# Performance work log

Hardware: AMD Instinct MI355X
Metric: run time of the kernel (lower is better)

Reference implementation:

```python
import jax, jax.numpy as jnp
import numpy as np

B, C, H, W, K = 8, 768, 64, 64, 256
EPS = 1e-12  # torch F.normalize eps


def setup_inputs() -> dict:
    key = jax.random.key(0)
    k1, k2 = jax.random.split(key)
    return {
        "x": jax.random.normal(k1, (B, C, H, W), dtype=jnp.float32),
        "centroids": jax.random.normal(k2, (B, C, K), dtype=jnp.float32),
        "sim_alpha": jnp.ones((1,), dtype=jnp.float32),
        "sim_beta": jnp.zeros((1,), dtype=jnp.float32),
    }


def reference(x, centroids, sim_alpha, sim_beta):
    b, c, h, w = x.shape
    n = h * w
    x_r = x.reshape(b, c, n)               # (B,C,N)
    xt = jnp.swapaxes(x_r, 1, 2)           # (B,N,C) tokens
    ct = jnp.swapaxes(centroids, 1, 2)     # (B,K,C) centroids
    # cosine similarity (F.normalize uses max(norm, eps))
    xn = xt / jnp.maximum(jnp.linalg.norm(xt, axis=-1, keepdims=True), EPS)
    cn = ct / jnp.maximum(jnp.linalg.norm(ct, axis=-1, keepdims=True), EPS)
    cos = jnp.einsum('bkc,bnc->bkn', cn, xn)                  # (B,K,N)
    sim = jax.nn.sigmoid(sim_beta + sim_alpha * cos)          # (B,K,N)
    # hard assignment mask: each token kept only for its argmax centroid
    max_idx = jnp.argmax(sim, axis=1)                         # (B,N)
    mask = jnp.swapaxes(jax.nn.one_hot(max_idx, sim.shape[1], dtype=sim.dtype), 1, 2)  # (B,K,N)
    sim_masked = sim * mask                                   # (B,K,N)
    # aggregation: sum over tokens weighted by masked similarity
    agg = jnp.einsum('bkn,bnc->bkc', sim_masked, xt)          # (B,K,C)
    counts = jnp.sum(mask, axis=-1, keepdims=True)            # (B,K,1)
    hyperedges = (agg + ct) / (counts + 1.0)                  # (B,K,C)
    return hyperedges, sim_masked
```

## Files before the change

### kernel.cpp

```cpp
#include <hip/hip_runtime.h>
#include <cmath>

#define Bdim 8
#define Cdim 768
#define Kdim 256
#define Ndim 4096
#define NT 64
#define KC2 32
#define NCH (Cdim / KC2)
#define CB2 4
#define NCOPY 4

typedef __bf16 bf16x8 __attribute__((ext_vector_type(8)));
typedef short  s16x8  __attribute__((ext_vector_type(8)));
typedef float  f32x4  __attribute__((ext_vector_type(4)));
union U8 { s16x8 s; bf16x8 b; };

typedef __attribute__((address_space(1))) const unsigned int g_u32;
typedef __attribute__((address_space(3))) unsigned int l_u32;
__device__ __forceinline__ void gload16(const void* g, void* l) {
    __builtin_amdgcn_global_load_lds((g_u32*)g, (l_u32*)l, 16, 0, 0);
}

__device__ __forceinline__ unsigned short bf16_rne(float f) {
    unsigned u = __float_as_uint(f);
    unsigned r = u + 0x7FFFu + ((u >> 16) & 1u);
    return (unsigned short)(r >> 16);
}
__device__ __forceinline__ float bf2f(unsigned short h) {
    return __uint_as_float((unsigned)h << 16);
}

__device__ __forceinline__ void lds_fadd_nc(float* p, float v) {
    auto lp = (__attribute__((address_space(3))) float*)p;
    asm volatile("ds_add_f32 %0, %1"
                 :: "v"((unsigned)(unsigned long long)lp), "v"(v));
}

__device__ __forceinline__ void split3(float v, short& h, short& m, short& l) {
    unsigned u = __float_as_uint(v);
    unsigned th = u + 0x7FFFu + ((u >> 16) & 1u);
    h = (short)(th >> 16);
    float r1 = v - __uint_as_float(th & 0xFFFF0000u);
    unsigned u1 = __float_as_uint(r1);
    unsigned tm = u1 + 0x7FFFu + ((u1 >> 16) & 1u);
    m = (short)(tm >> 16);
    float r2 = r1 - __uint_as_float(tm & 0xFFFF0000u);
    unsigned u2 = __float_as_uint(r2);
    unsigned tl = u2 + 0x7FFFu + ((u2 >> 16) & 1u);
    l = (short)(tl >> 16);
}

__global__ __launch_bounds__(256) void prep_kernel(
    const float* __restrict__ cents, float* __restrict__ invc, int* __restrict__ cnt)
{
    __shared__ float red[4][Kdim];
    const int tid = threadIdx.x;
    const int b = blockIdx.x;
    const float* cb = cents + (size_t)b * Cdim * Kdim;
    const int q = tid & 63, g = tid >> 6;
    float4 ss = make_float4(0.f, 0.f, 0.f, 0.f);
    for (int r = g; r < Cdim; r += 4) {
        float4 v = *(const float4*)(cb + (size_t)r * Kdim + q * 4);
        ss.x = fmaf(v.x, v.x, ss.x); ss.y = fmaf(v.y, v.y, ss.y);
        ss.z = fmaf(v.z, v.z, ss.z); ss.w = fmaf(v.w, v.w, ss.w);
    }
    *(float4*)&red[g][q * 4] = ss;
    __syncthreads();
    float s = red[0][tid] + red[1][tid] + red[2][tid] + red[3][tid];
    invc[b * Kdim + tid] = 1.f / fmaxf(sqrtf(s), 1e-12f);
    cnt[b * Kdim + tid] = 0;
}

__global__ __launch_bounds__(256) void cvt_kernel(
    const float* __restrict__ cents, short* __restrict__ centH,
    short* __restrict__ centM, short* __restrict__ centL)
{
    const int k = threadIdx.x;
    const int bc = blockIdx.x;
    const float* src = cents + ((size_t)(bc / 96) * Cdim + (size_t)(bc % 96) * 8) * Kdim + k;
    s16x8 H, M, L;
    #pragma unroll
    for (int e = 0; e < 8; ++e) {
        short h, m, l;
        split3(src[(size_t)e * Kdim], h, m, l);
        H[e] = h; M[e] = m; L[e] = l;
    }
    ((s16x8*)centH)[(size_t)bc * 256 + k] = H;
    ((s16x8*)centM)[(size_t)bc * 256 + k] = M;
    ((s16x8*)centL)[(size_t)bc * 256 + k] = L;
}

__global__ __launch_bounds__(256) void xpose_kernel(
    const float* __restrict__ x, unsigned short* __restrict__ xTh)
{
    __shared__ float tile[64][68];
    const int tid = threadIdx.x;
    const int bid = blockIdx.x;
    const int b  = bid / (12 * 64);
    const int r  = bid % (12 * 64);
    const int ct = r / 64, nt = r % 64;
    const float* src = x + ((size_t)b * Cdim + ct * 64) * Ndim + nt * 64;
    #pragma unroll
    for (int it = 0; it < 4; ++it) {
        int idx = tid + it * 256;
        int c = idx >> 4, n4 = idx & 15;
        float4 v = *(const float4*)&src[(size_t)c * Ndim + n4 * 4];
        *(float4*)&tile[c][n4 * 4] = v;
    }
    __syncthreads();
    #pragma unroll
    for (int it = 0; it < 8; ++it) {
        int idx = tid + it * 256;
        int n = idx >> 5, cp = idx & 31;
        unsigned pk = (unsigned)bf16_rne(tile[cp * 2][n])
                    | ((unsigned)bf16_rne(tile[cp * 2 + 1][n]) << 16);
        *(unsigned*)&xTh[((size_t)(b * Ndim + nt * 64 + n)) * Cdim + ct * 64 + cp * 2] = pk;
    }
}

__global__ __launch_bounds__(256) void scan_kernel(
    const int* __restrict__ cnt, const int* __restrict__ kArr,
    int* __restrict__ bucketOff, int* __restrict__ toks)
{
    __shared__ int cS[256];
    __shared__ int offS[256];
    __shared__ int cur[256];
    const int tid = threadIdx.x;
    const int b = blockIdx.x;
    cS[tid] = cnt[b * 256 + tid];
    __syncthreads();
    if (tid == 0) {
        int a = 0;
        for (int k = 0; k < 256; ++k) { offS[k] = a; a += cS[k]; }
    }
    __syncthreads();
    bucketOff[b * 256 + tid] = offS[tid];
    cur[tid] = offS[tid];
    __syncthreads();
    for (int i = tid; i < Ndim; i += 256) {
        int k = kArr[b * Ndim + i];
        int pos = atomicAdd(&cur[k], 1);
        toks[b * Ndim + pos] = i;
    }
}

__global__ __launch_bounds__(192) void aggB_kernel(
    const unsigned short* __restrict__ xTh,
    const float* __restrict__ cents,
    const float* __restrict__ wArr,
    const int* __restrict__ toks,
    const int* __restrict__ bucketOff,
    const int* __restrict__ cnt,
    float* __restrict__ hyp)
{
    const int tid = threadIdx.x;
    const int b  = blockIdx.x >> 7;
    const int kg = blockIdx.x & 127;
    const int t4 = tid * 4;
    #pragma unroll
    for (int j = 0; j < 2; ++j) {
        const int k = kg * 2 + j;
        const int off = bucketOff[b * 256 + k];
        const int num = cnt[b * 256 + k];
        const int base = b * Ndim + off;
        float a0 = 0.f, a1 = 0.f, a2 = 0.f, a3 = 0.f;
        int i = 0;
        for (; i + 4 <= num; i += 4) {
            int na = toks[base + i],     nb = toks[base + i + 1];
            int nc = toks[base + i + 2], nd = toks[base + i + 3];
            float wa = wArr[b * Ndim + na], wb = wArr[b * Ndim + nb];
            float wc = wArr[b * Ndim + nc], wd = wArr[b * Ndim + nd];
            ushort4 ha = *(const ushort4*)&xTh[((size_t)(b * Ndim + na)) * Cdim + t4];
            ushort4 hb = *(const ushort4*)&xTh[((size_t)(b * Ndim + nb)) * Cdim + t4];
            ushort4 hc = *(const ushort4*)&xTh[((size_t)(b * Ndim + nc)) * Cdim + t4];
            ushort4 hd = *(const ushort4*)&xTh[((size_t)(b * Ndim + nd)) * Cdim + t4];
            a0 += wa * bf2f(ha.x) + wb * bf2f(hb.x) + wc * bf2f(hc.x) + wd * bf2f(hd.x);
            a1 += wa * bf2f(ha.y) + wb * bf2f(hb.y) + wc * bf2f(hc.y) + wd * bf2f(hd.y);
            a2 += wa * bf2f(ha.z) + wb * bf2f(hb.z) + wc * bf2f(hc.z) + wd * bf2f(hd.z);
            a3 += wa * bf2f(ha.w) + wb * bf2f(hb.w) + wc * bf2f(hc.w) + wd * bf2f(hd.w);
        }
        for (; i < num; ++i) {
            int n = toks[base + i];
            float w = wArr[b * Ndim + n];
            ushort4 h = *(const ushort4*)&xTh[((size_t)(b * Ndim + n)) * Cdim + t4];
            a0 += w * bf2f(h.x); a1 += w * bf2f(h.y);
            a2 += w * bf2f(h.z); a3 += w * bf2f(h.w);
        }
        float d = (float)(num + 1);
        float4 o;
        o.x = (a0 + cents[((size_t)b * Cdim + t4 + 0) * Kdim + k]) / d;
        o.y = (a1 + cents[((size_t)b * Cdim + t4 + 1) * Kdim + k]) / d;
        o.z = (a2 + cents[((size_t)b * Cdim + t4 + 2) * Kdim + k]) / d;
        o.w = (a3 + cents[((size_t)b * Cdim + t4 + 3) * Kdim + k]) / d;
        *(float4*)&hyp[((size_t)(b * Kdim + k)) * Cdim + t4] = o;
    }
}

__global__ __launch_bounds__(256, 2) void sim_mfma_kernel(
    const float* __restrict__ x,
    const short* __restrict__ centH,
    const short* __restrict__ centM,
    const short* __restrict__ centL,
    const float* __restrict__ alpha_p,
    const float* __restrict__ beta_p,
    const float* __restrict__ invc,
    float* __restrict__ simOut,
    float* __restrict__ wArr,
    int*   __restrict__ kArr,
    int*   __restrict__ cnt)
{
    __shared__ __align__(16) float sxf[3][KC2][NT];
    __shared__ float invcS[Kdim];
    __shared__ float px[4][NT];
    __shared__ float invxS[NT];
    __shared__ float bwv[4][NT];
    __shared__ int   bwk[4][NT];

    const int tid  = threadIdx.x;
    const int lane = tid & 63;
    const int w    = tid >> 6;
    const int q    = lane >> 4;
    const int c15  = lane & 15;
    const int b    = blockIdx.x >> 6;
    const int n0   = (blockIdx.x & 63) * NT;
    const float* xb = x + (size_t)b * Cdim * Ndim;

    invcS[tid] = invc[b * Kdim + tid];
    const float alpha = alpha_p[0];
    const float beta  = beta_p[0];

    f32x4 acc[4][4];
    #pragma unroll
    for (int i = 0; i < 4; ++i)
        #pragma unroll
        for (int j = 0; j < 4; ++j) acc[i][j] = (f32x4){0.f, 0.f, 0.f, 0.f};

    float xn2p = 0.f;

    #define STAGE(t_) do {                                                    \
        const int bf_ = (t_) % 3; const int c0_ = (t_) * KC2;                 \
        _Pragma("unroll")                                                     \
        for (int i_ = 0; i_ < 2; ++i_)                                        \
            gload16(xb + (size_t)(c0_ + w * 8 + i_ * 4 + q) * Ndim            \
                       + n0 + c15 * 4,                                        \
                    &sxf[bf_][w * 8 + i_ * 4][0]);                            \
    } while (0)

    STAGE(0);
    STAGE(1);

    const s16x8* cHb = (const s16x8*)centH + ((size_t)b * 96) * 256;
    const s16x8* cMb = (const s16x8*)centM + ((size_t)b * 96) * 256;
    const s16x8* cLb = (const s16x8*)centL + ((size_t)b * 96) * 256;

    for (int t = 0; t < NCH; ++t) {
        asm volatile("s_waitcnt vmcnt(2)" ::: "memory");
        __builtin_amdgcn_s_barrier();
        __builtin_amdgcn_sched_barrier(0);

        const int cur = t % 3;

        U8 aH[4], aM[4], aL[4];
        {
            const size_t rowb = ((size_t)(t * 4 + q)) * 256 + w * 64 + c15;
            #pragma unroll
            for (int kf = 0; kf < 4; ++kf) {
                aH[kf].s = cHb[rowb + kf * 16];
                aM[kf].s = cMb[rowb + kf * 16];
                aL[kf].s = cLb[rowb + kf * 16];
            }
        }
        if (t + 2 < NCH) STAGE(t + 2);

        #pragma unroll
        for (int r = 0; r < 8; ++r) {
            float v = sxf[cur][w * 8 + r][lane];
            xn2p = fmaf(v, v, xn2p);
        }

        U8 bH[4], bM[4], bL[4];
        #pragma unroll
        for (int nf = 0; nf < 4; ++nf) {
            #pragma unroll
            for (int e = 0; e < 8; ++e) {
                short h, m, l;
                split3(sxf[cur][q * 8 + e][nf * 16 + c15], h, m, l);
                bH[nf].s[e] = h; bM[nf].s[e] = m; bL[nf].s[e] = l;
            }
        }

        #pragma unroll
        for (int kf = 0; kf < 4; ++kf)
            #pragma unroll
            for (int nf = 0; nf < 4; ++nf)
                acc[kf][nf] = __builtin_amdgcn_mfma_f32_16x16x32_bf16(
                    aH[kf].b, bH[nf].b, acc[kf][nf], 0, 0, 0);
        #pragma unroll
        for (int kf = 0; kf < 4; ++kf)
            #pragma unroll
            for (int nf = 0; nf < 4; ++nf)
                acc[kf][nf] = __builtin_amdgcn_mfma_f32_16x16x32_bf16(
                    aH[kf].b, bM[nf].b, acc[kf][nf], 0, 0, 0);
        #pragma unroll
        for (int kf = 0; kf < 4; ++kf)
            #pragma unroll
            for (int nf = 0; nf < 4; ++nf)
                acc[kf][nf] = __builtin_amdgcn_mfma_f32_16x16x32_bf16(
                    aM[kf].b, bH[nf].b, acc[kf][nf], 0, 0, 0);
        #pragma unroll
        for (int kf = 0; kf < 4; ++kf)
            #pragma unroll
            for (int nf = 0; nf < 4; ++nf)
                acc[kf][nf] = __builtin_amdgcn_mfma_f32_16x16x32_bf16(
                    aH[kf].b, bL[nf].b, acc[kf][nf], 0, 0, 0);
        #pragma unroll
        for (int kf = 0; kf < 4; ++kf)
            #pragma unroll
            for (int nf = 0; nf < 4; ++nf)
                acc[kf][nf] = __builtin_amdgcn_mfma_f32_16x16x32_bf16(
                    aL[kf].b, bH[nf].b, acc[kf][nf], 0, 0, 0);
        #pragma unroll
        for (int kf = 0; kf < 4; ++kf)
            #pragma unroll
            for (int nf = 0; nf < 4; ++nf)
                acc[kf][nf] = __builtin_amdgcn_mfma_f32_16x16x32_bf16(
                    aM[kf].b, bM[nf].b, acc[kf][nf], 0, 0, 0);
    }
    #undef STAGE

    __syncthreads();
    px[w][lane] = xn2p;
    __syncthreads();
    if (tid < NT) {
        float s = px[0][tid] + px[1][tid] + px[2][tid] + px[3][tid];
        invxS[tid] = 1.f / fmaxf(sqrtf(s), 1e-12f);
    }
    __syncthreads();

    #pragma unroll
    for (int nf = 0; nf < 4; ++nf) {
        const float ivx = invxS[nf * 16 + c15];
        float best = -1.f; int bk = 0;
        #pragma unroll
        for (int kf = 0; kf < 4; ++kf) {
            float4 ic = *(const float4*)&invcS[w * 64 + kf * 16 + q * 4];
            #pragma unroll
            for (int r = 0; r < 4; ++r) {
                float cosv = acc[kf][nf][r] * ((const float*)&ic)[r] * ivx;
                float s = 1.f / (1.f + expf(-(beta + alpha * cosv)));
                int k = w * 64 + kf * 16 + q * 4 + r;
                if (s > best) { best = s; bk = k; }
            }
        }
        #pragma unroll
        for (int off = 16; off < 64; off <<= 1) {
            float ov = __shfl_xor(best, off);
            int   ok = __shfl_xor(bk, off);
            if (ov > best || (ov == best && ok < bk)) { best = ov; bk = ok; }
        }
        if (q == 0) { bwv[w][nf * 16 + c15] = best; bwk[w][nf * 16 + c15] = bk; }
    }
    __syncthreads();
    if (tid < NT) {
        float best = -1.f; int bk = 0;
        #pragma unroll
        for (int g = 0; g < 4; ++g) {
            float v = bwv[g][tid];
            if (v > best) { best = v; bk = bwk[g][tid]; }
        }
        int gn = b * Ndim + n0 + tid;
        wArr[gn] = best;
        kArr[gn] = bk;
        simOut[((size_t)(b * Kdim + bk)) * Ndim + n0 + tid] = best;
        atomicAdd(&cnt[b * Kdim + bk], 1);
    }
}

__global__ __launch_bounds__(256, 4) void agg_kernel(
    const float* __restrict__ x, const float* __restrict__ cents,
    const float* __restrict__ wArr, const int* __restrict__ kArr,
    const int* __restrict__ cnt, float* __restrict__ hyp)
{
    __shared__ float accs[NCOPY][CB2][Kdim + 1];
    const int tid = threadIdx.x;
    const int b  = blockIdx.x / (Cdim / CB2);
    const int c0 = (blockIdx.x % (Cdim / CB2)) * CB2;
    const int cp = tid & 3;
    const float* xb = x + ((size_t)b * Cdim + c0) * Ndim;

    int4 kv[4]; float4 w4[4]; float4 xv[4][CB2];
    #pragma unroll
    for (int i = 0; i < 4; ++i) {
        const int n = (tid + i * 256) * 4;
        kv[i] = *(const int4*)&kArr[b * Ndim + n];
        w4[i] = *(const float4*)&wArr[b * Ndim + n];
        #pragma unroll
        for (int r = 0; r < CB2; ++r)
            xv[i][r] = *(const float4*)&xb[(size_t)r * Ndim + n];
    }
    for (int i = tid; i < NCOPY * CB2 * (Kdim + 1); i += 256) ((float*)accs)[i] = 0.f;
    __syncthreads();
    __builtin_amdgcn_sched_barrier(0);
    #pragma unroll
    for (int i = 0; i < 4; ++i)
        #pragma unroll
        for (int r = 0; r < CB2; ++r) {
            lds_fadd_nc(&accs[cp][r][kv[i].x], w4[i].x * xv[i][r].x);
            lds_fadd_nc(&accs[cp][r][kv[i].y], w4[i].y * xv[i][r].y);
            lds_fadd_nc(&accs[cp][r][kv[i].z], w4[i].z * xv[i][r].z);
            lds_fadd_nc(&accs[cp][r][kv[i].w], w4[i].w * xv[i][r].w);
        }
    asm volatile("s_waitcnt lgkmcnt(0)" ::: "memory");
    __builtin_amdgcn_sched_barrier(0);
    __syncthreads();
    const int cl = tid & 3;
    #pragma unroll
    for (int it = 0; it < 4; ++it) {
        int k = (tid >> 2) + it * 64;
        float s = accs[0][cl][k] + accs[1][cl][k] + accs[2][cl][k] + accs[3][cl][k];
        float num = s + cents[((size_t)b * Cdim + c0 + cl) * Kdim + k];
        hyp[((size_t)(b * Kdim + k)) * Cdim + c0 + cl] = num / (float)(cnt[b * Kdim + k] + 1);
    }
}

extern "C" void kernel_launch(void* const* d_in, const int* in_sizes, int n_in,
                              void* d_out, int out_size, void* d_ws, size_t ws_size,
                              hipStream_t stream)
{
    const float* x     = (const float*)d_in[0];
    const float* cents = (const float*)d_in[1];
    const float* alpha = (const float*)d_in[2];
    const float* beta  = (const float*)d_in[3];

    float* hyp    = (float*)d_out;
    float* simOut = (float*)d_out + (size_t)Bdim * Kdim * Cdim;

    char* ws = (char*)d_ws;
    float* wArr  = (float*)(ws);
    int*   kArr  = (int*)  (ws + 131072);
    int*   cnt   = (int*)  (ws + 262144);
    float* invc  = (float*)(ws + 270336);
    short* centH = (short*)(ws + 278528);
    short* centM = (short*)(ws + 3424256);
    short* centL = (short*)(ws + 6569984);
    int*   toks  = (int*)  (ws + 9715712);
    int*   boff  = (int*)  (ws + 9846784);
    unsigned short* xTh = (unsigned short*)(ws + 9854976);
    const size_t WS_NEED = 9854976ull + 50331648ull;

    hipMemsetAsync(simOut, 0, (size_t)Bdim * Kdim * Ndim * sizeof(float), stream);

    prep_kernel<<<dim3(Bdim), dim3(256), 0, stream>>>(cents, invc, cnt);
    cvt_kernel<<<dim3(Bdim * 96), dim3(256), 0, stream>>>(cents, centH, centM, centL);

    if (ws_size >= WS_NEED) {
        xpose_kernel<<<dim3(Bdim * 12 * 64), dim3(256), 0, stream>>>(x, xTh);
        sim_mfma_kernel<<<dim3(Bdim * (Ndim / NT)), dim3(256), 0, stream>>>(
            x, centH, centM, centL, alpha, beta, invc, simOut, wArr, kArr, cnt);
        scan_kernel<<<dim3(Bdim), dim3(256), 0, stream>>>(cnt, kArr, boff, toks);
        aggB_kernel<<<dim3(Bdim * 128), dim3(192), 0, stream>>>(
            xTh, cents, wArr, toks, boff, cnt, hyp);
    } else {
        sim_mfma_kernel<<<dim3(Bdim * (Ndim / NT)), dim3(256), 0, stream>>>(
            x, centH, centM, centL, alpha, beta, invc, simOut, wArr, kArr, cnt);
        agg_kernel<<<dim3(Bdim * (Cdim / CB2)), dim3(256), 0, stream>>>(
            x, cents, wArr, kArr, cnt, hyp);
    }
}
```

Measured before the change: 209.3 us.

## Pre-split x into transposed bf16 hi/mid/lo planes and read MFMA operands directly

A new transpose kernel splits x into three bf16 planes (high, mid, low) in token-major layout and writes per-chunk squared norms. A new similarity kernel then loads its MFMA operands straight from global memory without LDS staging or in-loop conversion, and sums the partial norms in its epilogue. The goal is to take the fp32-to-bf16x3 split and the LDS traffic out of the GEMM loop. The cost is a much larger workspace (about 150MB of x planes) plus extra global write and read traffic. The old fp32-x fallback and the agg_kernel are removed, so smaller workspaces now get no launches at all.

```diff
diff --git a/kernel.cpp b/kernel.cpp
--- a/kernel.cpp
+++ b/kernel.cpp
@@ -8,8 +8,6 @@
 #define NT 64
 #define KC2 32
 #define NCH (Cdim / KC2)
-#define CB2 4
-#define NCOPY 4
 
 typedef __bf16 bf16x8 __attribute__((ext_vector_type(8)));
 typedef short  s16x8  __attribute__((ext_vector_type(8)));
@@ -29,12 +27,6 @@
 }
 __device__ __forceinline__ float bf2f(unsigned short h) {
     return __uint_as_float((unsigned)h << 16);
-}
-
-__device__ __forceinline__ void lds_fadd_nc(float* p, float v) {
-    auto lp = (__attribute__((address_space(3))) float*)p;
-    asm volatile("ds_add_f32 %0, %1"
-                 :: "v"((unsigned)(unsigned long long)lp), "v"(v));
 }
 
 __device__ __forceinline__ void split3(float v, short& h, short& m, short& l) {
@@ -91,6 +83,56 @@
     ((s16x8*)centL)[(size_t)bc * 256 + k] = L;
 }
 
+__global__ __launch_bounds__(256) void xpose3_kernel(
+    const float* __restrict__ x,
+    unsigned short* __restrict__ xH, unsigned short* __restrict__ xM,
+    unsigned short* __restrict__ xL, float* __restrict__ xn2p)
+{
+    __shared__ float tile[64][68];
+    __shared__ float psum[4][64];
+    const int tid = threadIdx.x;
+    const int bid = blockIdx.x;
+    const int b  = bid / (12 * 64);
+    const int r  = bid % (12 * 64);
+    const int ct = r / 64, nt = r % 64;
+    const float* src = x + ((size_t)b * Cdim + ct * 64) * Ndim + nt * 64;
+    #pragma unroll
+    for (int it = 0; it < 4; ++it) {
+        int idx = tid + it * 256;
+        int c = idx >> 4, n4 = idx & 15;
+        *(float4*)&tile[c][n4 * 4] = *(const float4*)&src[(size_t)c * Ndim + n4 * 4];
+    }
+    __syncthreads();
+
+    {
+        const int grp = tid >> 6, tn = tid & 63;
+        float s = 0.f;
+        #pragma unroll
+        for (int cc = 0; cc < 16; ++cc) {
+            float v = tile[grp * 16 + cc][tn];
+            s = fmaf(v, v, s);
+        }
+        psum[grp][tn] = s;
+    }
+    __syncthreads();
+    if (tid < 64)
+        xn2p[((size_t)(b * 12 + ct)) * Ndim + nt * 64 + tid] =
+            psum[0][tid] + psum[1][tid] + psum[2][tid] + psum[3][tid];
+
+    #pragma unroll
+    for (int it = 0; it < 8; ++it) {
+        int idx = tid + it * 256;
+        int n = idx >> 5, cp = idx & 31;
+        short h0, m0, l0, h1, m1, l1;
+        split3(tile[cp * 2][n],     h0, m0, l0);
+        split3(tile[cp * 2 + 1][n], h1, m1, l1);
+        size_t o = ((size_t)(b * Ndim + nt * 64 + n)) * Cdim + ct * 64 + cp * 2;
+        *(unsigned*)&xH[o] = (unsigned)(unsigned short)h0 | ((unsigned)(unsigned short)h1 << 16);
+        *(unsigned*)&xM[o] = (unsigned)(unsigned short)m0 | ((unsigned)(unsigned short)m1 << 16);
+        *(unsigned*)&xL[o] = (unsigned)(unsigned short)l0 | ((unsigned)(unsigned short)l1 << 16);
+    }
+}
+
 __global__ __launch_bounds__(256) void xpose_kernel(
     const float* __restrict__ x, unsigned short* __restrict__ xTh)
 {
@@ -105,8 +147,7 @@
     for (int it = 0; it < 4; ++it) {
         int idx = tid + it * 256;
         int c = idx >> 4, n4 = idx & 15;
-        float4 v = *(const float4*)&src[(size_t)c * Ndim + n4 * 4];
-        *(float4*)&tile[c][n4 * 4] = v;
+        *(float4*)&tile[c][n4 * 4] = *(const float4*)&src[(size_t)c * Ndim + n4 * 4];
     }
     __syncthreads();
     #pragma unroll
@@ -197,6 +238,121 @@
     }
 }
 
+#define PASS(Afr, Bfr)                                                        \
+    _Pragma("unroll")                                                         \
+    for (int kf = 0; kf < 4; ++kf)                                            \
+        _Pragma("unroll")                                                     \
+        for (int nf = 0; nf < 4; ++nf)                                        \
+            acc[kf][nf] = __builtin_amdgcn_mfma_f32_16x16x32_bf16(            \
+                Afr[kf].b, Bfr[nf].b, acc[kf][nf], 0, 0, 0);
+
+__global__ __launch_bounds__(256, 2) void sim_direct_kernel(
+    const short* __restrict__ xH, const short* __restrict__ xM,
+    const short* __restrict__ xL,
+    const short* __restrict__ centH, const short* __restrict__ centM,
+    const short* __restrict__ centL,
+    const float* __restrict__ alpha_p, const float* __restrict__ beta_p,
+    const float* __restrict__ invc, const float* __restrict__ xn2p,
+    float* __restrict__ simOut, float* __restrict__ wArr,
+    int* __restrict__ kArr, int* __restrict__ cnt)
+{
+    __shared__ float bwv[4][NT];
+    __shared__ int   bwk[4][NT];
+
+    const int tid  = threadIdx.x;
+    const int lane = tid & 63;
+    const int w    = tid >> 6;
+    const int q    = lane >> 4;
+    const int c15  = lane & 15;
+    const int b    = blockIdx.x >> 6;
+    const int n0   = (blockIdx.x & 63) * NT;
+
+    const s16x8* xHb = (const s16x8*)xH;
+    const s16x8* xMb = (const s16x8*)xM;
+    const s16x8* xLb = (const s16x8*)xL;
+    size_t rB[4];
+    #pragma unroll
+    for (int nf = 0; nf < 4; ++nf)
+        rB[nf] = ((size_t)b * Ndim + n0 + nf * 16 + c15) * 96 + q;
+
+    const s16x8* cHb = (const s16x8*)centH + (size_t)b * 96 * 256;
+    const s16x8* cMb = (const s16x8*)centM + (size_t)b * 96 * 256;
+    const s16x8* cLb = (const s16x8*)centL + (size_t)b * 96 * 256;
+    const int rowA0 = w * 64 + c15;
+
+    f32x4 acc[4][4];
+    #pragma unroll
+    for (int i = 0; i < 4; ++i)
+        #pragma unroll
+        for (int j = 0; j < 4; ++j) acc[i][j] = (f32x4){0.f, 0.f, 0.f, 0.f};
+
+    #pragma unroll 1
+    for (int t = 0; t < NCH; ++t) {
+        U8 bH[4], bM[4], bL[4], aH[4], aM[4], aL[4];
+        #pragma unroll
+        for (int nf = 0; nf < 4; ++nf) bH[nf].s = xHb[rB[nf] + t * 4];
+        #pragma unroll
+        for (int nf = 0; nf < 4; ++nf) bM[nf].s = xMb[rB[nf] + t * 4];
+        #pragma unroll
+        for (int nf = 0; nf < 4; ++nf) bL[nf].s = xLb[rB[nf] + t * 4];
+        const int ra = (t * 4 + q) * 256 + rowA0;
+        #pragma unroll
+        for (int kf = 0; kf < 4; ++kf) aH[kf].s = cHb[ra + kf * 16];
+        #pragma unroll
+        for (int kf = 0; kf < 4; ++kf) aM[kf].s = cMb[ra + kf * 16];
+        #pragma unroll
+        for (int kf = 0; kf < 4; ++kf) aL[kf].s = cLb[ra + kf * 16];
+
+        PASS(aH, bH) PASS(aM, bH) PASS(aL, bH)
+        PASS(aH, bM) PASS(aM, bM) PASS(aH, bL)
+    }
+
+    const float alpha = alpha_p[0];
+    const float beta  = beta_p[0];
+
+    #pragma unroll
+    for (int nf = 0; nf < 4; ++nf) {
+        const int n = n0 + nf * 16 + c15;
+        float xs = 0.f;
+        #pragma unroll
+        for (int j = 0; j < 12; ++j) xs += xn2p[(size_t)(b * 12 + j) * Ndim + n];
+        const float ivx = 1.f / fmaxf(sqrtf(xs), 1e-12f);
+        float best = -1.f; int bk = 0;
+        #pragma unroll
+        for (int kf = 0; kf < 4; ++kf) {
+            float4 ic = *(const float4*)&invc[b * Kdim + w * 64 + kf * 16 + q * 4];
+            #pragma unroll
+            for (int r = 0; r < 4; ++r) {
+                float cosv = acc[kf][nf][r] * ((const float*)&ic)[r] * ivx;
+                float s = 1.f / (1.f + expf(-(beta + alpha * cosv)));
+                int k = w * 64 + kf * 16 + q * 4 + r;
+                if (s > best) { best = s; bk = k; }
+            }
+        }
+        #pragma unroll
+        for (int off = 16; off < 64; off <<= 1) {
+            float ov = __shfl_xor(best, off);
+            int   ok = __shfl_xor(bk, off);
+            if (ov > best || (ov == best && ok < bk)) { best = ov; bk = ok; }
+        }
+        if (q == 0) { bwv[w][nf * 16 + c15] = best; bwk[w][nf * 16 + c15] = bk; }
+    }
+    __syncthreads();
+    if (tid < NT) {
+        float best = -1.f; int bk = 0;
+        #pragma unroll
+        for (int g = 0; g < 4; ++g) {
+            float v = bwv[g][tid];
+            if (v > best) { best = v; bk = bwk[g][tid]; }
+        }
+        int gn = b * Ndim + n0 + tid;
+        wArr[gn] = best;
+        kArr[gn] = bk;
+        simOut[((size_t)(b * Kdim + bk)) * Ndim + n0 + tid] = best;
+        atomicAdd(&cnt[b * Kdim + bk], 1);
+    }
+}
+
 __global__ __launch_bounds__(256, 2) void sim_mfma_kernel(
     const float* __restrict__ x,
     const short* __restrict__ centH,
@@ -236,7 +392,7 @@
         #pragma unroll
         for (int j = 0; j < 4; ++j) acc[i][j] = (f32x4){0.f, 0.f, 0.f, 0.f};
 
-    float xn2p = 0.f;
+    float xn2p_ = 0.f;
 
     #define STAGE(t_) do {                                                    \
         const int bf_ = (t_) % 3; const int c0_ = (t_) * KC2;                 \
@@ -276,7 +432,7 @@
         #pragma unroll
         for (int r = 0; r < 8; ++r) {
             float v = sxf[cur][w * 8 + r][lane];
-            xn2p = fmaf(v, v, xn2p);
+            xn2p_ = fmaf(v, v, xn2p_);
         }
 
         U8 bH[4], bM[4], bL[4];
@@ -290,47 +446,13 @@
             }
         }
 
-        #pragma unroll
-        for (int kf = 0; kf < 4; ++kf)
-            #pragma unroll
-            for (int nf = 0; nf < 4; ++nf)
-                acc[kf][nf] = __builtin_amdgcn_mfma_f32_16x16x32_bf16(
-                    aH[kf].b, bH[nf].b, acc[kf][nf], 0, 0, 0);
-        #pragma unroll
-        for (int kf = 0; kf < 4; ++kf)
-            #pragma unroll
-            for (int nf = 0; nf < 4; ++nf)
-                acc[kf][nf] = __builtin_amdgcn_mfma_f32_16x16x32_bf16(
-                    aH[kf].b, bM[nf].b, acc[kf][nf], 0, 0, 0);
-        #pragma unroll
-        for (int kf = 0; kf < 4; ++kf)
-            #pragma unroll
-            for (int nf = 0; nf < 4; ++nf)
-                acc[kf][nf] = __builtin_amdgcn_mfma_f32_16x16x32_bf16(
-                    aM[kf].b, bH[nf].b, acc[kf][nf], 0, 0, 0);
-        #pragma unroll
-        for (int kf = 0; kf < 4; ++kf)
-            #pragma unroll
-            for (int nf = 0; nf < 4; ++nf)
-                acc[kf][nf] = __builtin_amdgcn_mfma_f32_16x16x32_bf16(
-                    aH[kf].b, bL[nf].b, acc[kf][nf], 0, 0, 0);
-        #pragma unroll
-        for (int kf = 0; kf < 4; ++kf)
-            #pragma unroll
-            for (int nf = 0; nf < 4; ++nf)
-                acc[kf][nf] = __builtin_amdgcn_mfma_f32_16x16x32_bf16(
-                    aL[kf].b, bH[nf].b, acc[kf][nf], 0, 0, 0);
-        #pragma unroll
-        for (int kf = 0; kf < 4; ++kf)
-            #pragma unroll
-            for (int nf = 0; nf < 4; ++nf)
-                acc[kf][nf] = __builtin_amdgcn_mfma_f32_16x16x32_bf16(
-                    aM[kf].b, bM[nf].b, acc[kf][nf], 0, 0, 0);
+        PASS(aH, bH) PASS(aH, bM) PASS(aM, bH)
+        PASS(aH, bL) PASS(aL, bH) PASS(aM, bM)
     }
     #undef STAGE
 
     __syncthreads();
-    px[w][lane] = xn2p;
+    px[w][lane] = xn2p_;
     __syncthreads();
     if (tid < NT) {
         float s = px[0][tid] + px[1][tid] + px[2][tid] + px[3][tid];
@@ -377,53 +499,6 @@
     }
 }
 
-__global__ __launch_bounds__(256, 4) void agg_kernel(
-    const float* __restrict__ x, const float* __restrict__ cents,
-    const float* __restrict__ wArr, const int* __restrict__ kArr,
-    const int* __restrict__ cnt, float* __restrict__ hyp)
-{
-    __shared__ float accs[NCOPY][CB2][Kdim + 1];
-    const int tid = threadIdx.x;
-    const int b  = blockIdx.x / (Cdim / CB2);
-    const int c0 = (blockIdx.x % (Cdim / CB2)) * CB2;
-    const int cp = tid & 3;
-    const float* xb = x + ((size_t)b * Cdim + c0) * Ndim;
-
-    int4 kv[4]; float4 w4[4]; float4 xv[4][CB2];
-    #pragma unroll
-    for (int i = 0; i < 4; ++i) {
-        const int n = (tid + i * 256) * 4;
-        kv[i] = *(const int4*)&kArr[b * Ndim + n];
-        w4[i] = *(const float4*)&wArr[b * Ndim + n];
-        #pragma unroll
-        for (int r = 0; r < CB2; ++r)
-            xv[i][r] = *(const float4*)&xb[(size_t)r * Ndim + n];
-    }
-    for (int i = tid; i < NCOPY * CB2 * (Kdim + 1); i += 256) ((float*)accs)[i] = 0.f;
-    __syncthreads();
-    __builtin_amdgcn_sched_barrier(0);
-    #pragma unroll
-    for (int i = 0; i < 4; ++i)
-        #pragma unroll
-        for (int r = 0; r < CB2; ++r) {
-            lds_fadd_nc(&accs[cp][r][kv[i].x], w4[i].x * xv[i][r].x);
-            lds_fadd_nc(&accs[cp][r][kv[i].y], w4[i].y * xv[i][r].y);
-            lds_fadd_nc(&accs[cp][r][kv[i].z], w4[i].z * xv[i][r].z);
-            lds_fadd_nc(&accs[cp][r][kv[i].w], w4[i].w * xv[i][r].w);
-        }
-    asm volatile("s_waitcnt lgkmcnt(0)" ::: "memory");
-    __builtin_amdgcn_sched_barrier(0);
-    __syncthreads();
-    const int cl = tid & 3;
-    #pragma unroll
-    for (int it = 0; it < 4; ++it) {
-        int k = (tid >> 2) + it * 64;
-        float s = accs[0][cl][k] + accs[1][cl][k] + accs[2][cl][k] + accs[3][cl][k];
-        float num = s + cents[((size_t)b * Cdim + c0 + cl) * Kdim + k];
-        hyp[((size_t)(b * Kdim + k)) * Cdim + c0 + cl] = num / (float)(cnt[b * Kdim + k] + 1);
-    }
-}
-
 extern "C" void kernel_launch(void* const* d_in, const int* in_sizes, int n_in,
                               void* d_out, int out_size, void* d_ws, size_t ws_size,
                               hipStream_t stream)
@@ -437,34 +512,55 @@
     float* simOut = (float*)d_out + (size_t)Bdim * Kdim * Cdim;
 
     char* ws = (char*)d_ws;
-    float* wArr  = (float*)(ws);
-    int*   kArr  = (int*)  (ws + 131072);
-    int*   cnt   = (int*)  (ws + 262144);
-    float* invc  = (float*)(ws + 270336);
-    short* centH = (short*)(ws + 278528);
-    short* centM = (short*)(ws + 3424256);
-    short* centL = (short*)(ws + 6569984);
-    int*   toks  = (int*)  (ws + 9715712);
-    int*   boff  = (int*)  (ws + 9846784);
-    unsigned short* xTh = (unsigned short*)(ws + 9854976);
-    const size_t WS_NEED = 9854976ull + 50331648ull;
-
     hipMemsetAsync(simOut, 0, (size_t)Bdim * Kdim * Ndim * sizeof(float), stream);
 
-    prep_kernel<<<dim3(Bdim), dim3(256), 0, stream>>>(cents, invc, cnt);
-    cvt_kernel<<<dim3(Bdim * 96), dim3(256), 0, stream>>>(cents, centH, centM, centL);
-
-    if (ws_size >= WS_NEED) {
+    const size_t WS_FULL = 162422784ull;
+    const size_t WS_R13  = 60186624ull;
+
+    if (ws_size >= WS_FULL) {
+        float* wArr  = (float*)(ws);
+        int*   kArr  = (int*)  (ws + 131072);
+        int*   cnt   = (int*)  (ws + 262144);
+        float* invc  = (float*)(ws + 270336);
+        float* xn2p  = (float*)(ws + 278528);
+        short* centH = (short*)(ws + 1851392);
+        short* centM = (short*)(ws + 4997120);
+        short* centL = (short*)(ws + 8142848);
+        int*   toks  = (int*)  (ws + 11288576);
+        int*   boff  = (int*)  (ws + 11419648);
+        unsigned short* xH = (unsigned short*)(ws + 11427840);
+        unsigned short* xM = (unsigned short*)(ws + 61759488);
+        unsigned short* xL = (unsigned short*)(ws + 112091136);
+
+        prep_kernel<<<dim3(Bdim), dim3(256), 0, stream>>>(cents, invc, cnt);
+        cvt_kernel<<<dim3(Bdim * 96), dim3(256), 0, stream>>>(cents, centH, centM, centL);
+        xpose3_kernel<<<dim3(Bdim * 12 * 64), dim3(256), 0, stream>>>(x, xH, xM, xL, xn2p);
+        sim_direct_kernel<<<dim3(Bdim * (Ndim / NT)), dim3(256), 0, stream>>>(
+            (const short*)xH, (const short*)xM, (const short*)xL,
+            centH, centM, centL, alpha, beta, invc, xn2p,
+            simOut, wArr, kArr, cnt);
+        scan_kernel<<<dim3(Bdim), dim3(256), 0, stream>>>(cnt, kArr, boff, toks);
+        aggB_kernel<<<dim3(Bdim * 128), dim3(192), 0, stream>>>(
+            xH, cents, wArr, toks, boff, cnt, hyp);
+    } else if (ws_size >= WS_R13) {
+        float* wArr  = (float*)(ws);
+        int*   kArr  = (int*)  (ws + 131072);
+        int*   cnt   = (int*)  (ws + 262144);
+        float* invc  = (float*)(ws + 270336);
+        short* centH = (short*)(ws + 278528);
+        short* centM = (short*)(ws + 3424256);
+        short* centL = (short*)(ws + 6569984);
+        int*   toks  = (int*)  (ws + 9715712);
+        int*   boff  = (int*)  (ws + 9846784);
+        unsigned short* xTh = (unsigned short*)(ws + 9854976);
+
+        prep_kernel<<<dim3(Bdim), dim3(256), 0, stream>>>(cents, invc, cnt);
+        cvt_kernel<<<dim3(Bdim * 96), dim3(256), 0, stream>>>(cents, centH, centM, centL);
         xpose_kernel<<<dim3(Bdim * 12 * 64), dim3(256), 0, stream>>>(x, xTh);
         sim_mfma_kernel<<<dim3(Bdim * (Ndim / NT)), dim3(256), 0, stream>>>(
             x, centH, centM, centL, alpha, beta, invc, simOut, wArr, kArr, cnt);
         scan_kernel<<<dim3(Bdim), dim3(256), 0, stream>>>(cnt, kArr, boff, toks);
         aggB_kernel<<<dim3(Bdim * 128), dim3(192), 0, stream>>>(
             xTh, cents, wArr, toks, boff, cnt, hyp);
-    } else {
-        sim_mfma_kernel<<<dim3(Bdim * (Ndim / NT)), dim3(256), 0, stream>>>(
-            x, centH, centM, centL, alpha, beta, invc, simOut, wArr, kArr, cnt);
-        agg_kernel<<<dim3(Bdim * (Cdim / CB2)), dim3(256), 0, stream>>>(
-            x, cents, wArr, kArr, cnt, hyp);
-    }
-}
+    }
+}
```

New measurement: 238.9 us. 14.1% more time.
